# Optimization experiments

Hardware: AMD Instinct MI355X
Metric: run time of the kernel (lower is better)

## Reference

```python
import jax, jax.numpy as jnp
import numpy as np

D_MODEL = 1024
N_HEADS = 16
D_HEAD = 64
LAMBDA_INIT = 0.8  # paper: 0.8 - 0.6*exp(-0.3*(layer-1)); layer=1 -> 0.8


def setup_inputs() -> dict:
    key = jax.random.key(0)
    ks = jax.random.split(key, 6)
    B, S = 2, 2048
    std = 0.02
    x = jax.random.normal(ks[0], (B, S, D_MODEL), dtype=jnp.float32)
    Wq = jax.random.normal(ks[1], (D_MODEL, 2 * N_HEADS * D_HEAD), dtype=jnp.float32) * std
    Wk = jax.random.normal(ks[2], (D_MODEL, 2 * N_HEADS * D_HEAD), dtype=jnp.float32) * std
    Wv = jax.random.normal(ks[3], (D_MODEL, 2 * N_HEADS * D_HEAD), dtype=jnp.float32) * std
    Wo = jax.random.normal(ks[4], (N_HEADS * D_HEAD, D_MODEL), dtype=jnp.float32) * std
    # lambda params initialized to zeros per source (lambda_q1 = zeros(d_head))
    lq1 = jnp.zeros((D_HEAD,), dtype=jnp.float32)
    lk1 = jnp.zeros((D_HEAD,), dtype=jnp.float32)
    lq2 = jnp.zeros((D_HEAD,), dtype=jnp.float32)
    lk2 = jnp.zeros((D_HEAD,), dtype=jnp.float32)
    return {"x": x, "Wq": Wq, "Wk": Wk, "Wv": Wv, "Wo": Wo,
            "lq1": lq1, "lk1": lk1, "lq2": lq2, "lk2": lk2}


def reference(x, Wq, Wk, Wv, Wo, lq1, lk1, lq2, lk2):
    B, S, D = x.shape
    h, dh = N_HEADS, D_HEAD
    # project and split into the two attention-map groups: [B, S, 2, h, dh]
    q = (x @ Wq).reshape(B, S, 2, h, dh)
    k = (x @ Wk).reshape(B, S, 2, h, dh)
    v = (x @ Wv).reshape(B, S, 2, h, dh)
    q1, q2 = q[:, :, 0], q[:, :, 1]  # [B, S, h, dh]
    k1, k2 = k[:, :, 0], k[:, :, 1]
    v1, v2 = v[:, :, 0], v[:, :, 1]

    scale = 1.0 / jnp.sqrt(jnp.asarray(dh, dtype=x.dtype))
    lam = jnp.exp(jnp.dot(lq1, lk1)) - jnp.exp(jnp.dot(lq2, lk2)) + LAMBDA_INIT

    causal = jnp.tril(jnp.ones((S, S), dtype=bool))  # [S, S]
    neg_inf = jnp.asarray(-1e30, dtype=x.dtype)

    s1 = jnp.einsum('bshd,bthd->bhst', q1, k1) * scale
    s2 = jnp.einsum('bshd,bthd->bhst', q2, k2) * scale
    s1 = jnp.where(causal, s1, neg_inf)
    s2 = jnp.where(causal, s2, neg_inf)
    a1 = jax.nn.softmax(s1, axis=-1)
    a2 = jax.nn.softmax(s2, axis=-1)

    # differential attention output per head: A1 @ V1 - lambda * (A2 @ V2)
    o = jnp.einsum('bhst,bthd->bshd', a1, v1) - lam * jnp.einsum('bhst,bthd->bshd', a2, v2)
    o = o.reshape(B, S, h * dh) * (1.0 - LAMBDA_INIT)
    return o @ Wo
```

## Files before the change

### kernel.cpp

```cpp
#include <hip/hip_runtime.h>
#include <hip/hip_bf16.h>

typedef __bf16 bf16_t;
typedef bf16_t bf16x8 __attribute__((ext_vector_type(8)));
typedef float f32x4 __attribute__((ext_vector_type(4)));
typedef float f32x16 __attribute__((ext_vector_type(16)));

static __device__ __forceinline__ f32x4 mfma16(bf16x8 a, bf16x8 b, f32x4 c) {
  return __builtin_amdgcn_mfma_f32_16x16x32_bf16(a, b, c, 0, 0, 0);
}
static __device__ __forceinline__ f32x16 mfma32(bf16x8 a, bf16x8 b, f32x16 c) {
  return __builtin_amdgcn_mfma_f32_32x32x16_bf16(a, b, c, 0, 0, 0);
}

static __device__ __forceinline__ void gload_lds16(const bf16_t* g, bf16_t* l) {
  __builtin_amdgcn_global_load_lds(
      (const __attribute__((address_space(1))) void*)g,
      (__attribute__((address_space(3))) void*)l, 16, 0, 0);
}

static __device__ __forceinline__ unsigned pkbf(float a, float b) {
  union { bf16_t h[2]; unsigned u; } p;
  p.h[0] = (bf16_t)a; p.h[1] = (bf16_t)b;
  return p.u;
}
static __device__ __forceinline__ void pl32swap(unsigned& a, unsigned& b) {
  asm volatile("v_permlane32_swap_b32 %0, %1" : "+v"(a), "+v"(b));
}


__global__ __launch_bounds__(64) void lam_kernel(const float* __restrict__ lq1,
                                                 const float* __restrict__ lk1,
                                                 const float* __restrict__ lq2,
                                                 const float* __restrict__ lk2,
                                                 float* __restrict__ lamp) {
  int l = threadIdx.x;
  float a = lq1[l] * lk1[l];
  float b = lq2[l] * lk2[l];
  #pragma unroll
  for (int msk = 32; msk; msk >>= 1) {
    a += __shfl_xor(a, msk);
    b += __shfl_xor(b, msk);
  }
  if (l == 0) lamp[0] = __expf(a) - __expf(b) + 0.8f;
}

__global__ __launch_bounds__(256) void cvt_x_kernel(const float* __restrict__ x,
                                                    bf16_t* __restrict__ xb) {
  int i = (blockIdx.x * 256 + threadIdx.x) * 4;
  float4 v = *reinterpret_cast<const float4*>(x + i);
  union { bf16_t h[4]; uint2 u; } pk;
  pk.h[0] = (bf16_t)v.x; pk.h[1] = (bf16_t)v.y;
  pk.h[2] = (bf16_t)v.z; pk.h[3] = (bf16_t)v.w;
  *reinterpret_cast<uint2*>(xb + i) = pk.u;
}

__global__ __launch_bounds__(256) void transpose_cvt(const float* __restrict__ W,
                                                     bf16_t* __restrict__ Wt,
                                                     int K, int N) {
  __shared__ float tile[32][33];
  int n0 = blockIdx.x * 32, k0 = blockIdx.y * 32;
  int x = threadIdx.x, y = threadIdx.y;
  #pragma unroll
  for (int i = 0; i < 32; i += 8)
    tile[y + i][x] = W[(size_t)(k0 + y + i) * N + n0 + x];
  __syncthreads();
  #pragma unroll
  for (int i = 0; i < 32; i += 8)
    Wt[(size_t)(n0 + y + i) * K + k0 + x] = (bf16_t)tile[x][y + i];
}


template <typename OutT>
static __device__ __forceinline__ void gemm_bt_body(const bf16_t* __restrict__ A,
                                                    const bf16_t* __restrict__ Bt,
                                                    OutT* __restrict__ C,
                                                    int M, int N, int K,
                                                    bool vtrans) {
  __shared__ bf16_t As[128 * 32];
  __shared__ bf16_t Bs[128 * 32];
  const int tid = threadIdx.x;
  const int w = tid >> 6, lane = tid & 63;
  const int g = lane >> 4, l15 = lane & 15;
  const int wm = w >> 1, wn = w & 1;
  const int rowBase = blockIdx.y * 128, colBase = blockIdx.x * 128;

  const int c0 = 2 * w, c1 = 2 * w + 1;
  const int srow0 = 16 * c0 + (lane >> 2);
  const int srow1 = 16 * c1 + (lane >> 2);
  const int scol = (lane & 3) * 8;

  f32x4 acc[4][4] = {};

  for (int k0 = 0; k0 < K; k0 += 32) {
    __syncthreads();
    gload_lds16(A + (size_t)(rowBase + srow0) * K + k0 + scol, &As[c0 * 512]);
    gload_lds16(A + (size_t)(rowBase + srow1) * K + k0 + scol, &As[c1 * 512]);
    gload_lds16(Bt + (size_t)(colBase + srow0) * K + k0 + scol, &Bs[c0 * 512]);
    gload_lds16(Bt + (size_t)(colBase + srow1) * K + k0 + scol, &Bs[c1 * 512]);
    __syncthreads();

    bf16x8 bfr[4];
    #pragma unroll
    for (int j = 0; j < 4; ++j)
      bfr[j] = *reinterpret_cast<const bf16x8*>(&Bs[(wn * 64 + j * 16 + l15) * 32 + g * 8]);
    #pragma unroll
    for (int i = 0; i < 4; ++i) {
      bf16x8 afr = *reinterpret_cast<const bf16x8*>(&As[(wm * 64 + i * 16 + l15) * 32 + g * 8]);
      #pragma unroll
      for (int j = 0; j < 4; ++j)
        acc[i][j] = mfma16(afr, bfr[j], acc[i][j]);
    }
  }

  if (vtrans) {
    #pragma unroll
    for (int i = 0; i < 4; ++i) {
      #pragma unroll
      for (int j = 0; j < 4; ++j) {
        int row = rowBase + wm * 64 + i * 16 + 4 * g;
        int col = colBase + wn * 64 + j * 16 + l15;
        int bb = row >> 11, s = row & 2047;
        union { bf16_t h[4]; uint2 u; } pk;
        #pragma unroll
        for (int r = 0; r < 4; ++r) pk.h[r] = (bf16_t)acc[i][j][r];
        *reinterpret_cast<uint2*>(
            (bf16_t*)C + ((size_t)bb * 2048 + col) * 2048 + s) = pk.u;
      }
    }
  } else {
    #pragma unroll
    for (int i = 0; i < 4; ++i) {
      #pragma unroll
      for (int j = 0; j < 4; ++j) {
        int row = rowBase + wm * 64 + i * 16 + 4 * g;
        int col = colBase + wn * 64 + j * 16 + l15;
        #pragma unroll
        for (int r = 0; r < 4; ++r)
          C[(size_t)(row + r) * N + col] = (OutT)acc[i][j][r];
      }
    }
  }
}

__global__ __launch_bounds__(256) void gemm_qkv(const bf16_t* __restrict__ xb,
                                                const bf16_t* __restrict__ Wqt,
                                                const bf16_t* __restrict__ Wkt,
                                                const bf16_t* __restrict__ Wvt,
                                                bf16_t* __restrict__ Q,
                                                bf16_t* __restrict__ K,
                                                bf16_t* __restrict__ Vtg) {
  const bf16_t* Bt = (blockIdx.z == 0) ? Wqt : (blockIdx.z == 1) ? Wkt : Wvt;
  bf16_t* C = (blockIdx.z == 0) ? Q : (blockIdx.z == 1) ? K : Vtg;
  gemm_bt_body<bf16_t>(xb, Bt, C, 4096, 2048, 1024, blockIdx.z == 2);
}

__global__ __launch_bounds__(256) void gemm_out(const bf16_t* __restrict__ Ob,
                                                const bf16_t* __restrict__ Wot,
                                                float* __restrict__ out) {
  gemm_bt_body<float>(Ob, Wot, out, 4096, 1024, 1024, false);
}


__global__ __launch_bounds__(256, 2)
void attn_kernel(const bf16_t* __restrict__ Qg, const bf16_t* __restrict__ Kg,
                 const bf16_t* __restrict__ Vtg, bf16_t* __restrict__ Og,
                 const float* __restrict__ lamp) {
  __shared__ bf16_t lds0[16384];
  __shared__ bf16_t lds1[16384];
  __shared__ float lsArr[4][2][32];

  const int tid = threadIdx.x;
  const int w = tid >> 6, lane = tid & 63;
  const int l31 = lane & 31, hi = lane >> 5;
  const int sw7 = l31 & 7;
  const int bx = blockIdx.x;
  const int tile = 15 - (bx >> 5);
  const int bh = bx & 31;
  const int b = bh >> 4, h = bh & 15;
  const int rowB = b * 2048;
  const int q0 = tile * 128;
  const float lam = *lamp;
  const float cexp = 0.125f * 1.44269504088896340736f;

  const int lk = lane >> 3;
  const int swc = (lane & 7) ^ (lk & 7);
  const int compw = w & 1;
  const size_t kbase = (size_t)(rowB + lk) * 2048 + compw * 1024 + h * 64 + swc * 8;
  const size_t vbase = ((size_t)b * 2048 + compw * 1024 + h * 64 + lk) * 2048 + swc * 8;

  auto stage = [&](bf16_t* buf, int j0) {
    char* bufb = (char*)buf;
    if (w < 2) {
      const bf16_t* src = Kg + kbase + (size_t)j0 * 2048;
      #pragma unroll
      for (int t = 0; t < 8; ++t)
        gload_lds16(src + (size_t)t * (8 * 2048),
                    (bf16_t*)(bufb + (w * 8 + t) * 1024));
    } else {
      const bf16_t* src = Vtg + vbase + j0;
      #pragma unroll
      for (int t = 0; t < 8; ++t)
        gload_lds16(src + (size_t)t * (8 * 2048),
                    (bf16_t*)(bufb + (w * 8 + t) * 1024));
    }
  };

  const int qg = q0 + w * 32 + l31;
  bf16x8 qf[2][4];
  #pragma unroll
  for (int comp = 0; comp < 2; ++comp)
    #pragma unroll
    for (int s = 0; s < 4; ++s)
      qf[comp][s] = *reinterpret_cast<const bf16x8*>(
          Qg + (size_t)(rowB + qg) * 2048 + comp * 1024 + h * 64 + s * 16 + hi * 8);

  f32x16 o[2][2] = {};
  float ls[2] = {0.f, 0.f};
  const int jmax = q0 + 64;

  stage(lds0, 0);
  __syncthreads();

  int cur = 0;
  #pragma unroll 1
  for (int j0 = 0; j0 <= jmax; j0 += 64) {
    bf16_t* bc = cur ? lds1 : lds0;
    bf16_t* bn = cur ? lds0 : lds1;
    if (j0 < jmax) stage(bn, j0 + 64);

    const char* bufb = (const char*)bc;
    const bool maskt = (j0 + 63 > q0 + w * 32);

    #pragma unroll
    for (int comp = 0; comp < 2; ++comp) {
      const char* Kb = bufb + comp * 8192;
      f32x16 sA0 = {}, sA1 = {};
      #pragma unroll
      for (int s = 0; s < 4; ++s) {
        int xo = ((2 * s + hi) ^ sw7) << 4;
        bf16x8 k0 = *reinterpret_cast<const bf16x8*>(Kb + l31 * 128 + xo);
        bf16x8 k1 = *reinterpret_cast<const bf16x8*>(Kb + (32 + l31) * 128 + xo);
        sA0 = mfma32(k0, qf[comp][s], sA0);
        sA1 = mfma32(k1, qf[comp][s], sA1);
      }
      float p0[16], p1[16];
      #pragma unroll
      for (int e = 0; e < 16; ++e) {
        float v0 = __builtin_exp2f(sA0[e] * cexp);
        float v1 = __builtin_exp2f(sA1[e] * cexp);
        if (maskt) {
          int krow = (e & 3) + 8 * (e >> 2) + 4 * hi;
          if (j0 + krow > qg) v0 = 0.f;
          if (j0 + 32 + krow > qg) v1 = 0.f;
        }
        p0[e] = v0; p1[e] = v1;
        ls[comp] += v0 + v1;
      }
      bf16x8 pa[4];
      #pragma unroll
      for (int sp = 0; sp < 2; ++sp) {
        {
          unsigned u0 = pkbf(p0[8 * sp + 0], p0[8 * sp + 1]);
          unsigned u1 = pkbf(p0[8 * sp + 2], p0[8 * sp + 3]);
          unsigned v0 = pkbf(p0[8 * sp + 4], p0[8 * sp + 5]);
          unsigned v1 = pkbf(p0[8 * sp + 6], p0[8 * sp + 7]);
          pl32swap(u0, v0);
          pl32swap(u1, v1);
          union { uint4 u; bf16x8 f; } cvt;
          cvt.u = make_uint4(u0, u1, v0, v1);
          pa[sp] = cvt.f;
        }
        {
          unsigned u0 = pkbf(p1[8 * sp + 0], p1[8 * sp + 1]);
          unsigned u1 = pkbf(p1[8 * sp + 2], p1[8 * sp + 3]);
          unsigned v0 = pkbf(p1[8 * sp + 4], p1[8 * sp + 5]);
          unsigned v1 = pkbf(p1[8 * sp + 6], p1[8 * sp + 7]);
          pl32swap(u0, v0);
          pl32swap(u1, v1);
          union { uint4 u; bf16x8 f; } cvt;
          cvt.u = make_uint4(u0, u1, v0, v1);
          pa[2 + sp] = cvt.f;
        }
      }
      const char* Vb = bufb + 16384 + comp * 8192;
      #pragma unroll
      for (int s = 0; s < 4; ++s) {
        int xo = ((2 * s + hi) ^ sw7) << 4;
        bf16x8 vf0 = *reinterpret_cast<const bf16x8*>(Vb + l31 * 128 + xo);
        bf16x8 vf1 = *reinterpret_cast<const bf16x8*>(Vb + (32 + l31) * 128 + xo);
        o[comp][0] = mfma32(pa[s], vf0, o[comp][0]);
        o[comp][1] = mfma32(pa[s], vf1, o[comp][1]);
      }
    }
    __syncthreads();
    cur ^= 1;
  }

  #pragma unroll
  for (int comp = 0; comp < 2; ++comp) {
    float tot = ls[comp] + __shfl_xor(ls[comp], 32);
    lsArr[w][comp][l31] = 1.f / tot;
  }
  #pragma unroll
  for (int e = 0; e < 16; ++e) {
    int ql = (e & 3) + 8 * (e >> 2) + 4 * hi;
    float i1 = lsArr[w][0][ql];
    float i2 = lsArr[w][1][ql] * lam;
    int row = rowB + q0 + w * 32 + ql;
    size_t rb = (size_t)row * 1024 + h * 64 + l31;
    Og[rb]      = (bf16_t)((o[0][0][e] * i1 - o[1][0][e] * i2) * 0.2f);
    Og[rb + 32] = (bf16_t)((o[0][1][e] * i1 - o[1][1][e] * i2) * 0.2f);
  }
}


extern "C" void kernel_launch(void* const* d_in, const int* in_sizes, int n_in,
                              void* d_out, int out_size, void* d_ws, size_t ws_size,
                              hipStream_t stream) {
  const float* x   = (const float*)d_in[0];
  const float* Wq  = (const float*)d_in[1];
  const float* Wk  = (const float*)d_in[2];
  const float* Wv  = (const float*)d_in[3];
  const float* Wo  = (const float*)d_in[4];
  const float* lq1 = (const float*)d_in[5];
  const float* lk1 = (const float*)d_in[6];
  const float* lq2 = (const float*)d_in[7];
  const float* lk2 = (const float*)d_in[8];
  float* out = (float*)d_out;

  char* ws = (char*)d_ws;
  size_t off = 0;
  auto alloc = [&](size_t bytes) -> char* {
    char* p = ws + off;
    off += (bytes + 255) & ~(size_t)255;
    return p;
  };
  bf16_t* xb  = (bf16_t*)alloc((size_t)4096 * 1024 * 2);
  bf16_t* Wqt = (bf16_t*)alloc((size_t)2048 * 1024 * 2);
  bf16_t* Wkt = (bf16_t*)alloc((size_t)2048 * 1024 * 2);
  bf16_t* Wvt = (bf16_t*)alloc((size_t)2048 * 1024 * 2);
  bf16_t* Wot = (bf16_t*)alloc((size_t)1024 * 1024 * 2);
  bf16_t* Qb  = (bf16_t*)alloc((size_t)4096 * 2048 * 2);
  bf16_t* Kb  = (bf16_t*)alloc((size_t)4096 * 2048 * 2);
  bf16_t* Vtg = (bf16_t*)alloc((size_t)4096 * 2048 * 2);
  bf16_t* Ob  = (bf16_t*)alloc((size_t)4096 * 1024 * 2);
  float*  lamp = (float*)alloc(256);

  lam_kernel<<<1, 64, 0, stream>>>(lq1, lk1, lq2, lk2, lamp);
  cvt_x_kernel<<<4096, 256, 0, stream>>>(x, xb);
  transpose_cvt<<<dim3(64, 32), dim3(32, 8), 0, stream>>>(Wq, Wqt, 1024, 2048);
  transpose_cvt<<<dim3(64, 32), dim3(32, 8), 0, stream>>>(Wk, Wkt, 1024, 2048);
  transpose_cvt<<<dim3(64, 32), dim3(32, 8), 0, stream>>>(Wv, Wvt, 1024, 2048);
  transpose_cvt<<<dim3(32, 32), dim3(32, 8), 0, stream>>>(Wo, Wot, 1024, 1024);
  gemm_qkv<<<dim3(16, 32, 3), 256, 0, stream>>>(xb, Wqt, Wkt, Wvt, Qb, Kb, Vtg);
  attn_kernel<<<512, 256, 0, stream>>>(Qb, Kb, Vtg, Ob, lamp);
  gemm_out<<<dim3(8, 32), 256, 0, stream>>>(Ob, Wot, out);
}
```

Measured before the change: 216.7 us.

## Pair causal query tiles per block, split keys across warp halves, swizzle GEMM blocks

Each attention block now uses 512 threads and handles two complementary causal query tiles (p and 15-p), so every block gets the same amount of work. Each step stages a 128-key chunk, and two groups of four warps each process half of it; their partial outputs and row sums are reduced through LDS in a finalize step. The QKV and output GEMMs also remap block indices so that consecutive blocks are spread across XCDs. The intent is to fix the causal load imbalance and tail effects, at the cost of more LDS (128KB), one block per CU, and extra sync and reduction work.

```diff
diff --git a/kernel.cpp b/kernel.cpp
--- a/kernel.cpp
+++ b/kernel.cpp
@@ -83,7 +83,12 @@
   const int w = tid >> 6, lane = tid & 63;
   const int g = lane >> 4, l15 = lane & 15;
   const int wm = w >> 1, wn = w & 1;
-  const int rowBase = blockIdx.y * 128, colBase = blockIdx.x * 128;
+
+  const int nbx = gridDim.x;
+  const int idx = blockIdx.y * nbx + blockIdx.x;
+  const int qq = (nbx * gridDim.y) >> 3;
+  const int sidx = (idx & 7) * qq + (idx >> 3);
+  const int rowBase = (sidx / nbx) * 128, colBase = (sidx % nbx) * 128;
 
   const int c0 = 2 * w, c1 = 2 * w + 1;
   const int srow0 = 16 * c0 + (lane >> 2);
@@ -162,155 +167,202 @@
 }
 
 
-__global__ __launch_bounds__(256, 2)
+__global__ __launch_bounds__(512, 1)
 void attn_kernel(const bf16_t* __restrict__ Qg, const bf16_t* __restrict__ Kg,
                  const bf16_t* __restrict__ Vtg, bf16_t* __restrict__ Og,
                  const float* __restrict__ lamp) {
-  __shared__ bf16_t lds0[16384];
-  __shared__ bf16_t lds1[16384];
+  __shared__ __align__(16) char ldsbuf[2][65536];
   __shared__ float lsArr[4][2][32];
 
   const int tid = threadIdx.x;
   const int w = tid >> 6, lane = tid & 63;
   const int l31 = lane & 31, hi = lane >> 5;
   const int sw7 = l31 & 7;
+  const int rowg = w & 3, keyh = w >> 2;
   const int bx = blockIdx.x;
-  const int tile = 15 - (bx >> 5);
+  const int p = bx >> 5;
   const int bh = bx & 31;
   const int b = bh >> 4, h = bh & 15;
   const int rowB = b * 2048;
-  const int q0 = tile * 128;
   const float lam = *lamp;
   const float cexp = 0.125f * 1.44269504088896340736f;
 
-  const int lk = lane >> 3;
-  const int swc = (lane & 7) ^ (lk & 7);
-  const int compw = w & 1;
-  const size_t kbase = (size_t)(rowB + lk) * 2048 + compw * 1024 + h * 64 + swc * 8;
-  const size_t vbase = ((size_t)b * 2048 + compw * 1024 + h * 64 + lk) * 2048 + swc * 8;
-
-  auto stage = [&](bf16_t* buf, int j0) {
-    char* bufb = (char*)buf;
-    if (w < 2) {
-      const bf16_t* src = Kg + kbase + (size_t)j0 * 2048;
+  const int lk8 = lane >> 3;
+  const int sc8 = (lane & 7) ^ lk8;
+  const int lk4 = lane >> 4;
+  const int wv = (w - 4) & 3;
+  const size_t kOff = (size_t)(rowB + ((w & 1) << 6) + lk8) * 2048 +
+                      (w >> 1) * 1024 + h * 64 + sc8 * 8;
+  const size_t vOff = ((size_t)b * 2048 + (wv >> 1) * 1024 + h * 64 +
+                       ((wv & 1) << 5) + lk4) * 2048;
+
+  auto stage = [&](char* bufb, int j0) {
+    if (w < 4) {
+      const bf16_t* src = Kg + kOff + (size_t)j0 * 2048;
+      char* dst = bufb + w * 8192;
       #pragma unroll
       for (int t = 0; t < 8; ++t)
-        gload_lds16(src + (size_t)t * (8 * 2048),
-                    (bf16_t*)(bufb + (w * 8 + t) * 1024));
+        gload_lds16(src + (size_t)t * (8 * 2048), (bf16_t*)(dst + t * 1024));
     } else {
-      const bf16_t* src = Vtg + vbase + j0;
-      #pragma unroll
-      for (int t = 0; t < 8; ++t)
-        gload_lds16(src + (size_t)t * (8 * 2048),
-                    (bf16_t*)(bufb + (w * 8 + t) * 1024));
+      const bf16_t* src = Vtg + vOff + j0;
+      char* dst = bufb + 32768 + wv * 8192;
+      #pragma unroll
+      for (int t = 0; t < 8; ++t) {
+        int sc16 = (lane & 15) ^ (((t & 1) << 2) + lk4);
+        gload_lds16(src + (size_t)t * (4 * 2048) + sc16 * 8,
+                    (bf16_t*)(dst + t * 1024));
+      }
     }
   };
 
-  const int qg = q0 + w * 32 + l31;
+  f32x16 o[2][2];
+  float ls[2];
   bf16x8 qf[2][4];
-  #pragma unroll
-  for (int comp = 0; comp < 2; ++comp)
+
+  auto sched_j0 = [&](int i) { return (i > p ? (i - p - 1) : i) << 7; };
+
+  auto finalize = [&](int q0, char* scratch) {
+    float* sf = (float*)scratch;
     #pragma unroll
-    for (int s = 0; s < 4; ++s)
-      qf[comp][s] = *reinterpret_cast<const bf16x8*>(
-          Qg + (size_t)(rowB + qg) * 2048 + comp * 1024 + h * 64 + s * 16 + hi * 8);
-
-  f32x16 o[2][2] = {};
-  float ls[2] = {0.f, 0.f};
-  const int jmax = q0 + 64;
-
-  stage(lds0, 0);
+    for (int rd = 0; rd < 4; ++rd) {
+      const int comp = rd >> 1, db = rd & 1;
+      __syncthreads();
+      if (w >= 4) {
+        float* bp = sf + (size_t)((w - 4) * 64 + lane) * 17;
+        #pragma unroll
+        for (int e = 0; e < 16; ++e) bp[e] = o[comp][db][e];
+        if (db == 0) bp[16] = ls[comp];
+      }
+      __syncthreads();
+      if (w < 4) {
+        const float* bp = sf + (size_t)(w * 64 + lane) * 17;
+        #pragma unroll
+        for (int e = 0; e < 16; ++e) o[comp][db][e] += bp[e];
+        if (db == 0) ls[comp] += bp[16];
+      }
+    }
+    __syncthreads();
+    if (w < 4) {
+      #pragma unroll
+      for (int comp = 0; comp < 2; ++comp) {
+        float tot = ls[comp] + __shfl_xor(ls[comp], 32);
+        lsArr[w][comp][l31] = 1.f / tot;
+      }
+    }
+    __syncthreads();
+    if (w < 4) {
+      #pragma unroll
+      for (int e = 0; e < 16; ++e) {
+        int ql = (e & 3) + 8 * (e >> 2) + 4 * hi;
+        float i1 = lsArr[w][0][ql];
+        float i2 = lsArr[w][1][ql] * lam;
+        int row = rowB + q0 + w * 32 + ql;
+        size_t rb = (size_t)row * 1024 + h * 64 + l31;
+        Og[rb]      = (bf16_t)((o[0][0][e] * i1 - o[1][0][e] * i2) * 0.2f);
+        Og[rb + 32] = (bf16_t)((o[0][1][e] * i1 - o[1][1][e] * i2) * 0.2f);
+      }
+    }
+  };
+
+  stage(ldsbuf[0], 0);
   __syncthreads();
 
-  int cur = 0;
   #pragma unroll 1
-  for (int j0 = 0; j0 <= jmax; j0 += 64) {
-    bf16_t* bc = cur ? lds1 : lds0;
-    bf16_t* bn = cur ? lds0 : lds1;
-    if (j0 < jmax) stage(bn, j0 + 64);
-
-    const char* bufb = (const char*)bc;
-    const bool maskt = (j0 + 63 > q0 + w * 32);
-
-    #pragma unroll
-    for (int comp = 0; comp < 2; ++comp) {
-      const char* Kb = bufb + comp * 8192;
-      f32x16 sA0 = {}, sA1 = {};
-      #pragma unroll
-      for (int s = 0; s < 4; ++s) {
-        int xo = ((2 * s + hi) ^ sw7) << 4;
-        bf16x8 k0 = *reinterpret_cast<const bf16x8*>(Kb + l31 * 128 + xo);
-        bf16x8 k1 = *reinterpret_cast<const bf16x8*>(Kb + (32 + l31) * 128 + xo);
-        sA0 = mfma32(k0, qf[comp][s], sA0);
-        sA1 = mfma32(k1, qf[comp][s], sA1);
-      }
-      float p0[16], p1[16];
-      #pragma unroll
-      for (int e = 0; e < 16; ++e) {
-        float v0 = __builtin_exp2f(sA0[e] * cexp);
-        float v1 = __builtin_exp2f(sA1[e] * cexp);
-        if (maskt) {
-          int krow = (e & 3) + 8 * (e >> 2) + 4 * hi;
-          if (j0 + krow > qg) v0 = 0.f;
-          if (j0 + 32 + krow > qg) v1 = 0.f;
+  for (int i = 0; i <= 16; ++i) {
+    const int q0 = (i > p ? 15 - p : p) << 7;
+    const int j0 = sched_j0(i);
+    char* bc = ldsbuf[i & 1];
+    char* bn = ldsbuf[(i + 1) & 1];
+    if (i < 16) stage(bn, sched_j0(i + 1));
+
+    if (i == 0 || i == p + 1) {
+      #pragma unroll
+      for (int comp = 0; comp < 2; ++comp)
+        #pragma unroll
+        for (int s = 0; s < 4; ++s)
+          qf[comp][s] = *reinterpret_cast<const bf16x8*>(
+              Qg + (size_t)(rowB + q0 + rowg * 32 + l31) * 2048 + comp * 1024 +
+              h * 64 + s * 16 + hi * 8);
+      #pragma unroll
+      for (int comp = 0; comp < 2; ++comp) {
+        o[comp][0] = (f32x16)0.f;
+        o[comp][1] = (f32x16)0.f;
+        ls[comp] = 0.f;
+      }
+    }
+
+    const int qg = q0 + rowg * 32 + l31;
+    const bool active = (j0 + keyh * 64) <= (q0 + rowg * 32 + 31);
+    if (active) {
+      const bool maskt = (j0 + keyh * 64 + 63) > (q0 + rowg * 32);
+      #pragma unroll
+      for (int comp = 0; comp < 2; ++comp) {
+        const char* Kb = bc + comp * 16384 + keyh * 64 * 128;
+        f32x16 sA0 = {}, sA1 = {};
+        #pragma unroll
+        for (int s = 0; s < 4; ++s) {
+          int xo = ((2 * s + hi) ^ sw7) << 4;
+          bf16x8 k0 = *reinterpret_cast<const bf16x8*>(Kb + l31 * 128 + xo);
+          bf16x8 k1 = *reinterpret_cast<const bf16x8*>(Kb + (32 + l31) * 128 + xo);
+          sA0 = mfma32(k0, qf[comp][s], sA0);
+          sA1 = mfma32(k1, qf[comp][s], sA1);
         }
-        p0[e] = v0; p1[e] = v1;
-        ls[comp] += v0 + v1;
-      }
-      bf16x8 pa[4];
-      #pragma unroll
-      for (int sp = 0; sp < 2; ++sp) {
-        {
-          unsigned u0 = pkbf(p0[8 * sp + 0], p0[8 * sp + 1]);
-          unsigned u1 = pkbf(p0[8 * sp + 2], p0[8 * sp + 3]);
-          unsigned v0 = pkbf(p0[8 * sp + 4], p0[8 * sp + 5]);
-          unsigned v1 = pkbf(p0[8 * sp + 6], p0[8 * sp + 7]);
-          pl32swap(u0, v0);
-          pl32swap(u1, v1);
-          union { uint4 u; bf16x8 f; } cvt;
-          cvt.u = make_uint4(u0, u1, v0, v1);
-          pa[sp] = cvt.f;
+        float p0[16], p1[16];
+        #pragma unroll
+        for (int e = 0; e < 16; ++e) {
+          float v0 = __builtin_exp2f(sA0[e] * cexp);
+          float v1 = __builtin_exp2f(sA1[e] * cexp);
+          if (maskt) {
+            int krow = (e & 3) + 8 * (e >> 2) + 4 * hi;
+            if (j0 + keyh * 64 + krow > qg) v0 = 0.f;
+            if (j0 + keyh * 64 + 32 + krow > qg) v1 = 0.f;
+          }
+          p0[e] = v0; p1[e] = v1;
+          ls[comp] += v0 + v1;
         }
-        {
-          unsigned u0 = pkbf(p1[8 * sp + 0], p1[8 * sp + 1]);
-          unsigned u1 = pkbf(p1[8 * sp + 2], p1[8 * sp + 3]);
-          unsigned v0 = pkbf(p1[8 * sp + 4], p1[8 * sp + 5]);
-          unsigned v1 = pkbf(p1[8 * sp + 6], p1[8 * sp + 7]);
-          pl32swap(u0, v0);
-          pl32swap(u1, v1);
-          union { uint4 u; bf16x8 f; } cvt;
-          cvt.u = make_uint4(u0, u1, v0, v1);
-          pa[2 + sp] = cvt.f;
+        bf16x8 pa[4];
+        #pragma unroll
+        for (int sp = 0; sp < 2; ++sp) {
+          {
+            unsigned u0 = pkbf(p0[8 * sp + 0], p0[8 * sp + 1]);
+            unsigned u1 = pkbf(p0[8 * sp + 2], p0[8 * sp + 3]);
+            unsigned v0 = pkbf(p0[8 * sp + 4], p0[8 * sp + 5]);
+            unsigned v1 = pkbf(p0[8 * sp + 6], p0[8 * sp + 7]);
+            pl32swap(u0, v0);
+            pl32swap(u1, v1);
+            union { uint4 u; bf16x8 f; } cvt;
+            cvt.u = make_uint4(u0, u1, v0, v1);
+            pa[sp] = cvt.f;
+          }
+          {
+            unsigned u0 = pkbf(p1[8 * sp + 0], p1[8 * sp + 1]);
+            unsigned u1 = pkbf(p1[8 * sp + 2], p1[8 * sp + 3]);
+            unsigned v0 = pkbf(p1[8 * sp + 4], p1[8 * sp + 5]);
+            unsigned v1 = pkbf(p1[8 * sp + 6], p1[8 * sp + 7]);
+            pl32swap(u0, v0);
+            pl32swap(u1, v1);
+            union { uint4 u; bf16x8 f; } cvt;
+            cvt.u = make_uint4(u0, u1, v0, v1);
+            pa[2 + sp] = cvt.f;
+          }
         }
-      }
-      const char* Vb = bufb + 16384 + comp * 8192;
-      #pragma unroll
-      for (int s = 0; s < 4; ++s) {
-        int xo = ((2 * s + hi) ^ sw7) << 4;
-        bf16x8 vf0 = *reinterpret_cast<const bf16x8*>(Vb + l31 * 128 + xo);
-        bf16x8 vf1 = *reinterpret_cast<const bf16x8*>(Vb + (32 + l31) * 128 + xo);
-        o[comp][0] = mfma32(pa[s], vf0, o[comp][0]);
-        o[comp][1] = mfma32(pa[s], vf1, o[comp][1]);
-      }
-    }
-    __syncthreads();
-    cur ^= 1;
-  }
-
-  #pragma unroll
-  for (int comp = 0; comp < 2; ++comp) {
-    float tot = ls[comp] + __shfl_xor(ls[comp], 32);
-    lsArr[w][comp][l31] = 1.f / tot;
-  }
-  #pragma unroll
-  for (int e = 0; e < 16; ++e) {
-    int ql = (e & 3) + 8 * (e >> 2) + 4 * hi;
-    float i1 = lsArr[w][0][ql];
-    float i2 = lsArr[w][1][ql] * lam;
-    int row = rowB + q0 + w * 32 + ql;
-    size_t rb = (size_t)row * 1024 + h * 64 + l31;
-    Og[rb]      = (bf16_t)((o[0][0][e] * i1 - o[1][0][e] * i2) * 0.2f);
-    Og[rb + 32] = (bf16_t)((o[0][1][e] * i1 - o[1][1][e] * i2) * 0.2f);
+        const char* Vb = bc + 32768 + comp * 16384;
+        #pragma unroll
+        for (int s = 0; s < 4; ++s) {
+          int sl = ((keyh * 8) | ((2 * s + hi) ^ sw7)) << 4;
+          bf16x8 vf0 = *reinterpret_cast<const bf16x8*>(Vb + l31 * 256 + sl);
+          bf16x8 vf1 = *reinterpret_cast<const bf16x8*>(Vb + (32 + l31) * 256 + sl);
+          o[comp][0] = mfma32(pa[s], vf0, o[comp][0]);
+          o[comp][1] = mfma32(pa[s], vf1, o[comp][1]);
+        }
+      }
+    }
+
+    if (i == p || i == 16) {
+      finalize(q0, bc);
+    } else {
+      __syncthreads();
+    }
   }
 }
 
@@ -354,6 +406,6 @@
   transpose_cvt<<<dim3(64, 32), dim3(32, 8), 0, stream>>>(Wv, Wvt, 1024, 2048);
   transpose_cvt<<<dim3(32, 32), dim3(32, 8), 0, stream>>>(Wo, Wot, 1024, 1024);
   gemm_qkv<<<dim3(16, 32, 3), 256, 0, stream>>>(xb, Wqt, Wkt, Wvt, Qb, Kb, Vtg);
-  attn_kernel<<<512, 256, 0, stream>>>(Qb, Kb, Vtg, Ob, lamp);
+  attn_kernel<<<256, 512, 0, stream>>>(Qb, Kb, Vtg, Ob, lamp);
   gemm_out<<<dim3(8, 32), 256, 0, stream>>>(Ob, Wot, out);
 }
```

Result: faster. 198.7 us (-8.3%).
